# Optimization experiments

Measured on AMD Instinct MI355X. Metric: run time of the kernel, lower is better.

Reference implementation:

```python
import math
import jax, jax.numpy as jnp
import numpy as np

D_MODEL = 1024
N_HEADS = 16
D_K = D_MODEL // N_HEADS


def _rope(x):
    """Interleaved rotary embedding, matching the torch stack/flatten layout.
    x: (b, h, s, d) with d even."""
    s, d = x.shape[2], x.shape[3]
    pos = jnp.arange(s, dtype=x.dtype)[:, None]                     # (s, 1)
    inv = 10000.0 ** (jnp.arange(0, d, 2, dtype=x.dtype) / d)       # (d/2,)
    theta = pos / inv                                               # (s, d/2)
    sin = jnp.repeat(jnp.sin(theta), 2, axis=-1)                    # (s, d)
    cos = jnp.repeat(jnp.cos(theta), 2, axis=-1)                    # (s, d)
    rot = jnp.stack([-x[..., 1::2], x[..., 0::2]], axis=-1).reshape(x.shape)
    return x * cos + rot * sin


def setup_inputs() -> dict:
    key = jax.random.key(0)
    ks = jax.random.split(key, 12)
    b, s, d = 2, 2048, D_MODEL
    sc = 1.0 / math.sqrt(d)
    inp = {
        "q": jax.random.normal(ks[0], (b, s, d), jnp.float32),
        "k": jax.random.normal(ks[1], (b, s, d), jnp.float32),
        "v": jax.random.normal(ks[2], (b, s, d), jnp.float32),
        "mask": jnp.ones((b, 1, 1, s), dtype=bool),
        "w_q": jax.random.normal(ks[3], (d, d), jnp.float32) * sc,
        "b_q": jnp.zeros((d,), jnp.float32),
        "w_k": jax.random.normal(ks[4], (d, d), jnp.float32) * sc,
        "b_k": jnp.zeros((d,), jnp.float32),
        "w_v": jax.random.normal(ks[5], (d, d), jnp.float32) * sc,
        "b_v": jnp.zeros((d,), jnp.float32),
        "w_o": jax.random.normal(ks[6], (d, d), jnp.float32) * sc,
        "b_o": jnp.zeros((d,), jnp.float32),
    }
    return inp


def reference(q, k, v, mask, w_q, b_q, w_k, b_k, w_v, b_v, w_o, b_o):
    b = q.shape[0]
    h, dk = N_HEADS, D_K
    # projections; w stored as (d_in, d_out)
    qh = (q @ w_q + b_q).reshape(b, -1, h, dk).transpose(0, 2, 1, 3)  # (b,h,s1,dk)
    kh = (k @ w_k + b_k).reshape(b, -1, h, dk).transpose(0, 2, 1, 3)  # (b,h,s2,dk)
    vh = (v @ w_v + b_v).reshape(b, -1, h, dk).transpose(0, 2, 1, 3)
    qh = _rope(qh)
    kh = _rope(kh)
    scores = jnp.einsum("bhqd,bhkd->bhqk", qh, kh) / math.sqrt(dk)
    scores = jnp.where(mask, scores, jnp.finfo(scores.dtype).min)
    attn = jax.nn.softmax(scores, axis=-1)
    out = jnp.einsum("bhqk,bhkd->bhqd", attn, vh)
    out = out.transpose(0, 2, 1, 3).reshape(b, -1, h * dk)
    return out @ w_o + b_o
```

## Files before the change

### kernel.cpp

```cpp
#include <hip/hip_runtime.h>

#define S_LEN 2048
#define DM 1024
#define NH 16

typedef __attribute__((ext_vector_type(8))) short short8;
typedef __attribute__((ext_vector_type(4))) float f32x4;
typedef __attribute__((ext_vector_type(4))) unsigned short ushort4v;

#define QSCALE 0.1803368801111204f

__device__ __forceinline__ unsigned short f2bf(float f) {
    unsigned int u = __float_as_uint(f);
    u += 0x7fffu + ((u >> 16) & 1u);
    return (unsigned short)(u >> 16);
}

__device__ __forceinline__ void gload16(const void* g, void* l) {
    __builtin_amdgcn_global_load_lds((const __attribute__((address_space(1))) void*)g,
                                     (__attribute__((address_space(3))) void*)l, 16, 0, 0);
}

__global__ __launch_bounds__(256) void trig_kernel(float* __restrict__ sin_t,
                                                   float* __restrict__ cos_t) {
    int idx = blockIdx.x * 256 + threadIdx.x;
    int pos = idx >> 5;
    int i = idx & 31;
    float theta = (float)pos / powf(10000.0f, (float)i * (1.0f / 32.0f));
    double t = (double)theta;
    sin_t[idx] = (float)sin(t);
    cos_t[idx] = (float)cos(t);
}

__global__ __launch_bounds__(256) void conv_kernel(const float* __restrict__ x,
                                                   unsigned short* __restrict__ y) {
    int i = (blockIdx.x * 256 + threadIdx.x) * 4;
    float4 v = *(const float4*)&x[i];
    ushort4v r;
    r.x = f2bf(v.x); r.y = f2bf(v.y); r.z = f2bf(v.z); r.w = f2bf(v.w);
    *(ushort4v*)&y[i] = r;
}

__global__ __launch_bounds__(256) void wtrans_kernel(const float* __restrict__ w,
                                                     unsigned short* __restrict__ wt) {
    __shared__ float tile[32][33];
    const int k0 = blockIdx.y * 32, n0 = blockIdx.x * 32;
    const int tx = threadIdx.x & 31, ty = threadIdx.x >> 5;
#pragma unroll
    for (int i = 0; i < 4; ++i)
        tile[ty + i * 8][tx] = w[(size_t)(k0 + ty + i * 8) * DM + n0 + tx];
    __syncthreads();
#pragma unroll
    for (int i = 0; i < 4; ++i)
        wt[(size_t)(n0 + ty + i * 8) * DM + k0 + tx] = f2bf(tile[tx][ty + i * 8]);
}

__global__ __launch_bounds__(256, 3) void mmqkv_kernel(
    const unsigned short* __restrict__ qb, const unsigned short* __restrict__ kb,
    const unsigned short* __restrict__ vb, const unsigned short* __restrict__ wT,
    const float* __restrict__ b_q, const float* __restrict__ b_k,
    const float* __restrict__ b_v, unsigned short* __restrict__ outbase,
    const float* __restrict__ sin_t, const float* __restrict__ cos_t) {
    __shared__ __align__(16) short As[8192];
    __shared__ __align__(16) short Bs[8192];
    const int z = blockIdx.z;
    const unsigned short* A = (z == 0) ? qb : (z == 1) ? kb : vb;
    const unsigned short* Bt = wT + (size_t)z * DM * DM;
    const float* bias = (z == 0) ? b_q : (z == 1) ? b_k : b_v;
    unsigned short* out = outbase + (size_t)z * 4096 * DM;

    const int t = threadIdx.x;
    const int lane = t & 63;
    const int w = t >> 6;
    const int wm = w & 1, wn = w >> 1;
    const int lg = lane >> 4, lr = lane & 15;
    const int n0 = blockIdx.x * 128, m0 = blockIdx.y * 128;

    const int srow = t >> 3;
    const int skb = ((t & 7) ^ ((t >> 3) & 7)) << 4;
    const char* Ab = (const char*)A + (size_t)m0 * 2048 + skb;
    const char* Bb = (const char*)Bt + (size_t)n0 * 2048 + skb;
    char* AsB = (char*)As;
    char* BsB = (char*)Bs;

    f32x4 acc[4][4];
#pragma unroll
    for (int i = 0; i < 4; ++i)
#pragma unroll
        for (int j = 0; j < 4; ++j)
#pragma unroll
            for (int e = 0; e < 4; ++e) acc[i][j][e] = 0.0f;

    for (int kb2 = 0; kb2 < 2048; kb2 += 128) {
#pragma unroll
        for (int i = 0; i < 4; ++i) {
            gload16(Ab + (size_t)(i * 32 + srow) * 2048 + kb2, AsB + i * 4096 + t * 16);
            gload16(Bb + (size_t)(i * 32 + srow) * 2048 + kb2, BsB + i * 4096 + t * 16);
        }
        __syncthreads();
#pragma unroll
        for (int ks = 0; ks < 2; ++ks) {
            short8 a[4], b[4];
#pragma unroll
            for (int mi = 0; mi < 4; ++mi) {
                const int ra = wm * 64 + mi * 16 + lr;
                a[mi] = *(const short8*)(AsB + ra * 128 + ((ks * 64 + lg * 16) ^ ((ra & 7) << 4)));
                const int rb = wn * 64 + mi * 16 + lr;
                b[mi] = *(const short8*)(BsB + rb * 128 + ((ks * 64 + lg * 16) ^ ((rb & 7) << 4)));
            }
#pragma unroll
            for (int mi = 0; mi < 4; ++mi)
#pragma unroll
                for (int ni = 0; ni < 4; ++ni)
                    acc[mi][ni] = __builtin_amdgcn_mfma_f32_16x16x32_bf16(
                        a[mi], b[ni], acc[mi][ni], 0, 0, 0);
        }
        __syncthreads();
    }

    const int colbase = n0 + wn * 64;
    const int rowbase = m0 + wm * 64;
    const bool do_rope = (z < 2);
#pragma unroll
    for (int ni = 0; ni < 4; ++ni) {
        const int col = colbase + ni * 16 + lr;
        const float bv = bias[col];
#pragma unroll
        for (int mi = 0; mi < 4; ++mi) {
#pragma unroll
            for (int r = 0; r < 4; ++r) {
                const int row = rowbase + mi * 16 + lg * 4 + r;
                float o = acc[mi][ni][r] + bv;
                if (do_rope) {
                    const int srw = row & (S_LEN - 1);
                    const int pi = (col & 63) >> 1;
                    const float sv = sin_t[srw * 32 + pi];
                    const float cv = cos_t[srw * 32 + pi];
                    const float partner = __shfl_xor(o, 1);
                    o = (lr & 1) ? (o * cv + partner * sv) : (o * cv - partner * sv);
                    if (z == 0) o *= QSCALE;
                }
                out[(size_t)row * DM + col] = f2bf(o);
            }
        }
    }
}

__global__ __launch_bounds__(256, 2) void mmo_kernel(
    const unsigned short* __restrict__ A, const unsigned short* __restrict__ Bt,
    const float* __restrict__ bias, float* __restrict__ out) {
    __shared__ __align__(16) short As[4096];
    __shared__ __align__(16) short Bs[8192];
    const int t = threadIdx.x;
    const int lane = t & 63;
    const int wn = t >> 6;
    const int lg = lane >> 4, lr = lane & 15;
    const int n0 = blockIdx.x * 128, m0 = blockIdx.y * 64;

    const int srow = t >> 3;
    const int skb = ((t & 7) ^ ((t >> 3) & 7)) << 4;
    const char* Ab = (const char*)A + (size_t)m0 * 2048 + skb;
    const char* Bb = (const char*)Bt + (size_t)n0 * 2048 + skb;
    char* AsB = (char*)As;
    char* BsB = (char*)Bs;

    f32x4 acc[4][2];
#pragma unroll
    for (int i = 0; i < 4; ++i)
#pragma unroll
        for (int j = 0; j < 2; ++j)
#pragma unroll
            for (int e = 0; e < 4; ++e) acc[i][j][e] = 0.0f;

    for (int kb2 = 0; kb2 < 2048; kb2 += 128) {
#pragma unroll
        for (int i = 0; i < 2; ++i)
            gload16(Ab + (size_t)(i * 32 + srow) * 2048 + kb2, AsB + i * 4096 + t * 16);
#pragma unroll
        for (int i = 0; i < 4; ++i)
            gload16(Bb + (size_t)(i * 32 + srow) * 2048 + kb2, BsB + i * 4096 + t * 16);
        __syncthreads();
#pragma unroll
        for (int ks = 0; ks < 2; ++ks) {
            short8 a[4], b[2];
#pragma unroll
            for (int mi = 0; mi < 4; ++mi) {
                const int ra = mi * 16 + lr;
                a[mi] = *(const short8*)(AsB + ra * 128 + ((ks * 64 + lg * 16) ^ ((ra & 7) << 4)));
            }
#pragma unroll
            for (int ni = 0; ni < 2; ++ni) {
                const int rb = wn * 32 + ni * 16 + lr;
                b[ni] = *(const short8*)(BsB + rb * 128 + ((ks * 64 + lg * 16) ^ ((rb & 7) << 4)));
            }
#pragma unroll
            for (int mi = 0; mi < 4; ++mi)
#pragma unroll
                for (int ni = 0; ni < 2; ++ni)
                    acc[mi][ni] = __builtin_amdgcn_mfma_f32_16x16x32_bf16(
                        a[mi], b[ni], acc[mi][ni], 0, 0, 0);
        }
        __syncthreads();
    }

#pragma unroll
    for (int ni = 0; ni < 2; ++ni) {
        const int col = n0 + wn * 32 + ni * 16 + lr;
        const float bv = bias[col];
#pragma unroll
        for (int mi = 0; mi < 4; ++mi)
#pragma unroll
            for (int r = 0; r < 4; ++r) {
                const int row = m0 + mi * 16 + lg * 4 + r;
                out[(size_t)row * DM + col] = acc[mi][ni][r] + bv;
            }
    }
}

__global__ __launch_bounds__(256, 4) void flash_kernel(
    const unsigned short* __restrict__ qh, const unsigned short* __restrict__ kh,
    const unsigned short* __restrict__ vh, unsigned short* __restrict__ att) {
    __shared__ __align__(16) short Ks[4096];
    __shared__ __align__(16) short Vt[64][72];
    __shared__ __align__(16) short Pl[4][16 * 72];
    const int t = threadIdx.x;
    const int lane = t & 63;
    const int w = t >> 6;
    const int lg = lane >> 4, lr = lane & 15;
    const int q0 = blockIdx.x * 64;
    const int b = blockIdx.y >> 4, h = blockIdx.y & 15;
    const char* qB = (const char*)qh + (size_t)b * S_LEN * 2048 + h * 128;
    const char* kB = (const char*)kh + (size_t)b * S_LEN * 2048 + h * 128;
    const char* vB = (const char*)vh + (size_t)b * S_LEN * 2048 + h * 128;

    short8 qf[2];
#pragma unroll
    for (int ks = 0; ks < 2; ++ks)
        qf[ks] = *(const short8*)(qB + (size_t)(q0 + w * 16 + lr) * 2048 + ks * 64 + lg * 16);

    short8 onesv;
#pragma unroll
    for (int j = 0; j < 8; ++j) onesv[j] = (short)0x3F80;

    f32x4 oa[5];
    float mrow[4];
#pragma unroll
    for (int r = 0; r < 4; ++r) {
        mrow[r] = -1e30f;
#pragma unroll
        for (int di = 0; di < 5; ++di) oa[di][r] = 0.0f;
    }

    const int srow = t >> 3;
    const int skb = ((t & 7) ^ ((t >> 3) & 7)) << 4;
    const int vkey = lane;
    const int vd0 = w * 16;
    char* PlB = (char*)&Pl[w][0];

    for (int kt = 0; kt < S_LEN; kt += 64) {
#pragma unroll
        for (int i = 0; i < 2; ++i)
            gload16(kB + (size_t)(kt + i * 32 + srow) * 2048 + skb,
                    (char*)Ks + i * 4096 + t * 16);
        const char* vrow = vB + (size_t)(kt + vkey) * 2048 + vd0 * 2;
        short8 v0 = *(const short8*)(vrow);
        short8 v1 = *(const short8*)(vrow + 16);
#pragma unroll
        for (int j = 0; j < 8; ++j) {
            Vt[vd0 + j][vkey] = v0[j];
            Vt[vd0 + 8 + j][vkey] = v1[j];
        }
        __syncthreads();

        f32x4 s[4];
#pragma unroll
        for (int ki = 0; ki < 4; ++ki)
#pragma unroll
            for (int e = 0; e < 4; ++e) s[ki][e] = 0.0f;
#pragma unroll
        for (int ks = 0; ks < 2; ++ks) {
            short8 kf[4];
#pragma unroll
            for (int ki = 0; ki < 4; ++ki) {
                const int key = ki * 16 + lr;
                kf[ki] = *(const short8*)((char*)Ks + key * 128 +
                                          ((ks * 64 + lg * 16) ^ ((key & 7) << 4)));
            }
            __builtin_amdgcn_s_setprio(1);
#pragma unroll
            for (int ki = 0; ki < 4; ++ki)
                s[ki] = __builtin_amdgcn_mfma_f32_16x16x32_bf16(qf[ks], kf[ki], s[ki], 0, 0, 0);
            __builtin_amdgcn_s_setprio(0);
        }

#pragma unroll
        for (int r = 0; r < 4; ++r) {
            float mx = fmaxf(fmaxf(s[0][r], s[1][r]), fmaxf(s[2][r], s[3][r]));
            mx = fmaxf(mx, __shfl_xor(mx, 1));
            mx = fmaxf(mx, __shfl_xor(mx, 2));
            mx = fmaxf(mx, __shfl_xor(mx, 4));
            mx = fmaxf(mx, __shfl_xor(mx, 8));
            const float mn = fmaxf(mrow[r], mx);
            const float corr = exp2f(mrow[r] - mn);
            mrow[r] = mn;
#pragma unroll
            for (int di = 0; di < 5; ++di) oa[di][r] *= corr;
            const int qrow = lg * 4 + r;
            const int xq = (qrow & 12) << 3;
#pragma unroll
            for (int ki = 0; ki < 4; ++ki)
                *(unsigned short*)(PlB + qrow * 144 + (((ki * 16 + lr) * 2) ^ xq)) =
                    f2bf(exp2f(s[ki][r] - mn));
        }
        asm volatile("s_waitcnt lgkmcnt(0)" ::: "memory");

#pragma unroll
        for (int ks = 0; ks < 2; ++ks) {
            short8 pf, vf[4];
            pf = *(const short8*)(PlB + lr * 144 + ((ks * 64 + lg * 16) ^ ((lr & 12) << 3)));
#pragma unroll
            for (int di = 0; di < 4; ++di)
                vf[di] = *(const short8*)((const char*)&Vt[di * 16 + lr][0] + ks * 64 + lg * 16);
            __builtin_amdgcn_s_setprio(1);
#pragma unroll
            for (int di = 0; di < 4; ++di)
                oa[di] = __builtin_amdgcn_mfma_f32_16x16x32_bf16(pf, vf[di], oa[di], 0, 0, 0);
            oa[4] = __builtin_amdgcn_mfma_f32_16x16x32_bf16(pf, onesv, oa[4], 0, 0, 0);
            __builtin_amdgcn_s_setprio(0);
        }
        __syncthreads();
    }

#pragma unroll
    for (int r = 0; r < 4; ++r) {
        const float inv = 1.0f / oa[4][r];
        const int row = q0 + w * 16 + lg * 4 + r;
#pragma unroll
        for (int di = 0; di < 4; ++di)
            att[(size_t)(b * S_LEN + row) * DM + h * 64 + di * 16 + lr] =
                f2bf(oa[di][r] * inv);
    }
}

extern "C" void kernel_launch(void* const* d_in, const int* in_sizes, int n_in,
                              void* d_out, int out_size, void* d_ws, size_t ws_size,
                              hipStream_t stream) {
    const float* q = (const float*)d_in[0];
    const float* k = (const float*)d_in[1];
    const float* v = (const float*)d_in[2];
    const float* w_q = (const float*)d_in[4];
    const float* b_q = (const float*)d_in[5];
    const float* w_k = (const float*)d_in[6];
    const float* b_k = (const float*)d_in[7];
    const float* w_v = (const float*)d_in[8];
    const float* b_v = (const float*)d_in[9];
    const float* w_o = (const float*)d_in[10];
    const float* b_o = (const float*)d_in[11];

    char* p = (char*)d_ws;
    const size_t SZ_ACT = (size_t)4096 * DM * 2;
    const size_t SZ_W = (size_t)DM * DM * 2;
    unsigned short* qb = (unsigned short*)p; p += SZ_ACT;
    unsigned short* kb = (unsigned short*)p; p += SZ_ACT;
    unsigned short* vb = (unsigned short*)p; p += SZ_ACT;
    unsigned short* wqkvT = (unsigned short*)p; p += 3 * SZ_W;
    unsigned short* woT = (unsigned short*)p; p += SZ_W;
    unsigned short* qkvh = (unsigned short*)p; p += 3 * SZ_ACT;
    unsigned short* attp = (unsigned short*)p; p += SZ_ACT;
    float* sin_t = (float*)p; p += (size_t)S_LEN * 32 * 4;
    float* cos_t = (float*)p;

    trig_kernel<<<dim3(S_LEN * 32 / 256), dim3(256), 0, stream>>>(sin_t, cos_t);
    conv_kernel<<<dim3(4096), dim3(256), 0, stream>>>(q, qb);
    conv_kernel<<<dim3(4096), dim3(256), 0, stream>>>(k, kb);
    conv_kernel<<<dim3(4096), dim3(256), 0, stream>>>(v, vb);
    dim3 tg(32, 32);
    wtrans_kernel<<<tg, dim3(256), 0, stream>>>(w_q, wqkvT);
    wtrans_kernel<<<tg, dim3(256), 0, stream>>>(w_k, wqkvT + (size_t)DM * DM);
    wtrans_kernel<<<tg, dim3(256), 0, stream>>>(w_v, wqkvT + (size_t)2 * DM * DM);
    wtrans_kernel<<<tg, dim3(256), 0, stream>>>(w_o, woT);

    mmqkv_kernel<<<dim3(DM / 128, 4096 / 128, 3), dim3(256), 0, stream>>>(
        qb, kb, vb, wqkvT, b_q, b_k, b_v, qkvh, sin_t, cos_t);

    unsigned short* qhp = qkvh;
    unsigned short* khp = qkvh + (size_t)4096 * DM;
    unsigned short* vhp = qkvh + (size_t)2 * 4096 * DM;
    flash_kernel<<<dim3(S_LEN / 64, 32), dim3(256), 0, stream>>>(qhp, khp, vhp, attp);

    mmo_kernel<<<dim3(DM / 128, 4096 / 64), dim3(256), 0, stream>>>(
        attp, woT, b_o, (float*)d_out);
}
```

Measured before the change: 304.3 us.

## Double-buffer flash attention, keep P in registers, remap block order, batch prep launches

The flash kernel now gives each block 128 query rows, double-buffers K and V tiles in LDS, and computes S transposed so the probabilities stay in registers and feed 16x16x16 MFMAs directly instead of going through LDS. It also rescales the running max lazily, only when a row max grows by more than a threshold. The QKV, output and flash kernels remap block IDs so neighbouring blocks land on different XCDs, and setprio is wrapped around the GEMM MFMAs. The conversion, transpose and trig launches are merged into batched grids, with sin and cos packed into float2. Fewer blocks per CU and higher register use may reduce occupancy.

```diff
diff --git a/kernel.cpp b/kernel.cpp
--- a/kernel.cpp
+++ b/kernel.cpp
@@ -5,6 +5,7 @@
 #define NH 16
 
 typedef __attribute__((ext_vector_type(8))) short short8;
+typedef __attribute__((ext_vector_type(4))) short short4v;
 typedef __attribute__((ext_vector_type(4))) float f32x4;
 typedef __attribute__((ext_vector_type(4))) unsigned short ushort4v;
 
@@ -21,29 +22,53 @@
                                      (__attribute__((address_space(3))) void*)l, 16, 0, 0);
 }
 
-__global__ __launch_bounds__(256) void trig_kernel(float* __restrict__ sin_t,
-                                                   float* __restrict__ cos_t) {
+#if __has_builtin(__builtin_amdgcn_mfma_f32_16x16x16bf16_1k)
+__device__ __forceinline__ f32x4 mfma16(short4v a, short4v b, f32x4 c) {
+    return __builtin_amdgcn_mfma_f32_16x16x16bf16_1k(a, b, c, 0, 0, 0);
+}
+#elif __has_builtin(__builtin_amdgcn_mfma_f32_16x16x16_bf16)
+__device__ __forceinline__ f32x4 mfma16(short4v a, short4v b, f32x4 c) {
+    return __builtin_amdgcn_mfma_f32_16x16x16_bf16(a, b, c, 0, 0, 0);
+}
+#else
+__device__ __forceinline__ f32x4 mfma16(short4v a, short4v b, f32x4 c) {
+    asm("v_mfma_f32_16x16x16_bf16 %0, %1, %2, %0" : "+v"(c) : "v"(a), "v"(b));
+    return c;
+}
+#endif
+
+__global__ __launch_bounds__(256) void trig_kernel(float2* __restrict__ cs_t) {
     int idx = blockIdx.x * 256 + threadIdx.x;
     int pos = idx >> 5;
     int i = idx & 31;
     float theta = (float)pos / powf(10000.0f, (float)i * (1.0f / 32.0f));
     double t = (double)theta;
-    sin_t[idx] = (float)sin(t);
-    cos_t[idx] = (float)cos(t);
-}
-
-__global__ __launch_bounds__(256) void conv_kernel(const float* __restrict__ x,
+    cs_t[idx] = make_float2((float)cos(t), (float)sin(t));
+}
+
+__global__ __launch_bounds__(256) void conv_kernel(const float* __restrict__ q,
+                                                   const float* __restrict__ k,
+                                                   const float* __restrict__ v,
                                                    unsigned short* __restrict__ y) {
+    const int z = blockIdx.y;
+    const float* x = (z == 0) ? q : (z == 1) ? k : v;
+    unsigned short* yz = y + (size_t)z * 4096 * DM;
     int i = (blockIdx.x * 256 + threadIdx.x) * 4;
-    float4 v = *(const float4*)&x[i];
+    float4 vv = *(const float4*)&x[i];
     ushort4v r;
-    r.x = f2bf(v.x); r.y = f2bf(v.y); r.z = f2bf(v.z); r.w = f2bf(v.w);
-    *(ushort4v*)&y[i] = r;
-}
-
-__global__ __launch_bounds__(256) void wtrans_kernel(const float* __restrict__ w,
+    r.x = f2bf(vv.x); r.y = f2bf(vv.y); r.z = f2bf(vv.z); r.w = f2bf(vv.w);
+    *(ushort4v*)&yz[i] = r;
+}
+
+__global__ __launch_bounds__(256) void wtrans_kernel(const float* __restrict__ w_q,
+                                                     const float* __restrict__ w_k,
+                                                     const float* __restrict__ w_v,
+                                                     const float* __restrict__ w_o,
                                                      unsigned short* __restrict__ wt) {
     __shared__ float tile[32][33];
+    const int z = blockIdx.z;
+    const float* w = (z == 0) ? w_q : (z == 1) ? w_k : (z == 2) ? w_v : w_o;
+    unsigned short* wtz = wt + (size_t)z * DM * DM;
     const int k0 = blockIdx.y * 32, n0 = blockIdx.x * 32;
     const int tx = threadIdx.x & 31, ty = threadIdx.x >> 5;
 #pragma unroll
@@ -52,19 +77,24 @@
     __syncthreads();
 #pragma unroll
     for (int i = 0; i < 4; ++i)
-        wt[(size_t)(n0 + ty + i * 8) * DM + k0 + tx] = f2bf(tile[tx][ty + i * 8]);
+        wtz[(size_t)(n0 + ty + i * 8) * DM + k0 + tx] = f2bf(tile[tx][ty + i * 8]);
 }
 
 __global__ __launch_bounds__(256, 3) void mmqkv_kernel(
-    const unsigned short* __restrict__ qb, const unsigned short* __restrict__ kb,
-    const unsigned short* __restrict__ vb, const unsigned short* __restrict__ wT,
+    const unsigned short* __restrict__ qkvb, const unsigned short* __restrict__ wT,
     const float* __restrict__ b_q, const float* __restrict__ b_k,
     const float* __restrict__ b_v, unsigned short* __restrict__ outbase,
-    const float* __restrict__ sin_t, const float* __restrict__ cos_t) {
+    const float2* __restrict__ cs_t) {
     __shared__ __align__(16) short As[8192];
     __shared__ __align__(16) short Bs[8192];
-    const int z = blockIdx.z;
-    const unsigned short* A = (z == 0) ? qb : (z == 1) ? kb : vb;
+
+    const int fid = blockIdx.x + (blockIdx.y << 3) + (blockIdx.z << 8);
+    const int sid = (fid & 7) * 96 + (fid >> 3);
+    const int z = sid >> 8;
+    const int m0 = ((sid >> 3) & 31) * 128;
+    const int n0 = (sid & 7) * 128;
+
+    const unsigned short* A = qkvb + (size_t)z * 4096 * DM;
     const unsigned short* Bt = wT + (size_t)z * DM * DM;
     const float* bias = (z == 0) ? b_q : (z == 1) ? b_k : b_v;
     unsigned short* out = outbase + (size_t)z * 4096 * DM;
@@ -74,7 +104,6 @@
     const int w = t >> 6;
     const int wm = w & 1, wn = w >> 1;
     const int lg = lane >> 4, lr = lane & 15;
-    const int n0 = blockIdx.x * 128, m0 = blockIdx.y * 128;
 
     const int srow = t >> 3;
     const int skb = ((t & 7) ^ ((t >> 3) & 7)) << 4;
@@ -108,12 +137,14 @@
                 const int rb = wn * 64 + mi * 16 + lr;
                 b[mi] = *(const short8*)(BsB + rb * 128 + ((ks * 64 + lg * 16) ^ ((rb & 7) << 4)));
             }
+            __builtin_amdgcn_s_setprio(1);
 #pragma unroll
             for (int mi = 0; mi < 4; ++mi)
 #pragma unroll
                 for (int ni = 0; ni < 4; ++ni)
                     acc[mi][ni] = __builtin_amdgcn_mfma_f32_16x16x32_bf16(
                         a[mi], b[ni], acc[mi][ni], 0, 0, 0);
+            __builtin_amdgcn_s_setprio(0);
         }
         __syncthreads();
     }
@@ -125,6 +156,7 @@
     for (int ni = 0; ni < 4; ++ni) {
         const int col = colbase + ni * 16 + lr;
         const float bv = bias[col];
+        const int pi = (col & 63) >> 1;
 #pragma unroll
         for (int mi = 0; mi < 4; ++mi) {
 #pragma unroll
@@ -133,11 +165,9 @@
                 float o = acc[mi][ni][r] + bv;
                 if (do_rope) {
                     const int srw = row & (S_LEN - 1);
-                    const int pi = (col & 63) >> 1;
-                    const float sv = sin_t[srw * 32 + pi];
-                    const float cv = cos_t[srw * 32 + pi];
+                    const float2 cs = cs_t[srw * 32 + pi];
                     const float partner = __shfl_xor(o, 1);
-                    o = (lr & 1) ? (o * cv + partner * sv) : (o * cv - partner * sv);
+                    o = (lr & 1) ? (o * cs.x + partner * cs.y) : (o * cs.x - partner * cs.y);
                     if (z == 0) o *= QSCALE;
                 }
                 out[(size_t)row * DM + col] = f2bf(o);
@@ -155,7 +185,10 @@
     const int lane = t & 63;
     const int wn = t >> 6;
     const int lg = lane >> 4, lr = lane & 15;
-    const int n0 = blockIdx.x * 128, m0 = blockIdx.y * 64;
+
+    const int fid = blockIdx.x + (blockIdx.y << 3);
+    const int sid = (fid & 7) * 64 + (fid >> 3);
+    const int n0 = (sid & 7) * 128, m0 = (sid >> 3) * 64;
 
     const int srow = t >> 3;
     const int skb = ((t & 7) ^ ((t >> 3) & 7)) << 4;
@@ -193,12 +226,14 @@
                 const int rb = wn * 32 + ni * 16 + lr;
                 b[ni] = *(const short8*)(BsB + rb * 128 + ((ks * 64 + lg * 16) ^ ((rb & 7) << 4)));
             }
+            __builtin_amdgcn_s_setprio(1);
 #pragma unroll
             for (int mi = 0; mi < 4; ++mi)
 #pragma unroll
                 for (int ni = 0; ni < 2; ++ni)
                     acc[mi][ni] = __builtin_amdgcn_mfma_f32_16x16x32_bf16(
                         a[mi], b[ni], acc[mi][ni], 0, 0, 0);
+            __builtin_amdgcn_s_setprio(0);
         }
         __syncthreads();
     }
@@ -217,129 +252,190 @@
     }
 }
 
-__global__ __launch_bounds__(256, 4) void flash_kernel(
+__global__ __launch_bounds__(256, 2) void flash_kernel(
     const unsigned short* __restrict__ qh, const unsigned short* __restrict__ kh,
     const unsigned short* __restrict__ vh, unsigned short* __restrict__ att) {
-    __shared__ __align__(16) short Ks[4096];
-    __shared__ __align__(16) short Vt[64][72];
-    __shared__ __align__(16) short Pl[4][16 * 72];
+    __shared__ __align__(16) short Ks[2][4096];
+    __shared__ __align__(16) short Vt[2][64][72];
     const int t = threadIdx.x;
     const int lane = t & 63;
     const int w = t >> 6;
     const int lg = lane >> 4, lr = lane & 15;
-    const int q0 = blockIdx.x * 64;
-    const int b = blockIdx.y >> 4, h = blockIdx.y & 15;
+
+    const int fid = blockIdx.x + (blockIdx.y << 4);
+    const int sid = (fid & 7) * 64 + (fid >> 3);
+    const int q0 = (sid & 15) * 128;
+    const int bh = sid >> 4;
+    const int b = bh >> 4, h = bh & 15;
+
     const char* qB = (const char*)qh + (size_t)b * S_LEN * 2048 + h * 128;
     const char* kB = (const char*)kh + (size_t)b * S_LEN * 2048 + h * 128;
     const char* vB = (const char*)vh + (size_t)b * S_LEN * 2048 + h * 128;
 
-    short8 qf[2];
-#pragma unroll
-    for (int ks = 0; ks < 2; ++ks)
-        qf[ks] = *(const short8*)(qB + (size_t)(q0 + w * 16 + lr) * 2048 + ks * 64 + lg * 16);
-
-    short8 onesv;
-#pragma unroll
-    for (int j = 0; j < 8; ++j) onesv[j] = (short)0x3F80;
-
-    f32x4 oa[5];
-    float mrow[4];
-#pragma unroll
-    for (int r = 0; r < 4; ++r) {
-        mrow[r] = -1e30f;
-#pragma unroll
-        for (int di = 0; di < 5; ++di) oa[di][r] = 0.0f;
-    }
+    short8 qf[2][2];
+#pragma unroll
+    for (int qi = 0; qi < 2; ++qi)
+#pragma unroll
+        for (int ks = 0; ks < 2; ++ks)
+            qf[qi][ks] = *(const short8*)(qB +
+                (size_t)(q0 + w * 32 + qi * 16 + lr) * 2048 + ks * 64 + lg * 16);
 
     const int srow = t >> 3;
-    const int skb = ((t & 7) ^ ((t >> 3) & 7)) << 4;
-    const int vkey = lane;
-    const int vd0 = w * 16;
-    char* PlB = (char*)&Pl[w][0];
-
-    for (int kt = 0; kt < S_LEN; kt += 64) {
-#pragma unroll
-        for (int i = 0; i < 2; ++i)
-            gload16(kB + (size_t)(kt + i * 32 + srow) * 2048 + skb,
-                    (char*)Ks + i * 4096 + t * 16);
-        const char* vrow = vB + (size_t)(kt + vkey) * 2048 + vd0 * 2;
-        short8 v0 = *(const short8*)(vrow);
-        short8 v1 = *(const short8*)(vrow + 16);
+    const int skb = ((t & 7) ^ (srow & 7)) << 4;
+    const int va = t & 31;
+    const int vdb = t >> 5;
+    const size_t vsrc0 = (size_t)(2 * va) * 2048 + vdb * 16;
+
+    f32x4 s[2][4], oa[2][4], oa4[2];
+    float mrow[2] = {-1e30f, -1e30f};
+#pragma unroll
+    for (int qi = 0; qi < 2; ++qi) {
+#pragma unroll
+        for (int e = 0; e < 4; ++e) oa4[qi][e] = 0.0f;
+#pragma unroll
+        for (int di = 0; di < 4; ++di)
+#pragma unroll
+            for (int e = 0; e < 4; ++e) oa[qi][di][e] = 0.0f;
+    }
+    short4v ones4;
+#pragma unroll
+    for (int j = 0; j < 4; ++j) ones4[j] = (short)0x3F80;
+
+    gload16(kB + (size_t)srow * 2048 + skb, (char*)Ks[0] + t * 16);
+    gload16(kB + (size_t)(32 + srow) * 2048 + skb, (char*)Ks[0] + 4096 + t * 16);
+    {
+        short8 a0 = *(const short8*)(vB + vsrc0);
+        short8 a1 = *(const short8*)(vB + vsrc0 + 2048);
 #pragma unroll
         for (int j = 0; j < 8; ++j) {
-            Vt[vd0 + j][vkey] = v0[j];
-            Vt[vd0 + 8 + j][vkey] = v1[j];
-        }
-        __syncthreads();
-
-        f32x4 s[4];
-#pragma unroll
-        for (int ki = 0; ki < 4; ++ki)
-#pragma unroll
-            for (int e = 0; e < 4; ++e) s[ki][e] = 0.0f;
+            unsigned d = (unsigned)(unsigned short)a0[j] |
+                         ((unsigned)(unsigned short)a1[j] << 16);
+            *(unsigned*)&Vt[0][vdb * 8 + j][va * 2] = d;
+        }
+    }
+    __syncthreads();
+
+    for (int it = 0; it < 32; ++it) {
+        const int cb = it & 1;
+        const char* ksB = (const char*)Ks[cb];
+        char* ksN = (char*)Ks[cb ^ 1];
+        const char* vC = (const char*)&Vt[cb][0][0];
+
+        short8 a0, a1;
+        if (it < 31) {
+            const size_t kt2 = (size_t)(it + 1) * 64;
+            gload16(kB + (kt2 + srow) * 2048 + skb, ksN + t * 16);
+            gload16(kB + (kt2 + 32 + srow) * 2048 + skb, ksN + 4096 + t * 16);
+            a0 = *(const short8*)(vB + kt2 * 2048 + vsrc0);
+            a1 = *(const short8*)(vB + kt2 * 2048 + vsrc0 + 2048);
+        }
+
+#pragma unroll
+        for (int qi = 0; qi < 2; ++qi)
+#pragma unroll
+            for (int ki = 0; ki < 4; ++ki)
+#pragma unroll
+                for (int e = 0; e < 4; ++e) s[qi][ki][e] = 0.0f;
 #pragma unroll
         for (int ks = 0; ks < 2; ++ks) {
             short8 kf[4];
 #pragma unroll
             for (int ki = 0; ki < 4; ++ki) {
                 const int key = ki * 16 + lr;
-                kf[ki] = *(const short8*)((char*)Ks + key * 128 +
+                kf[ki] = *(const short8*)(ksB + key * 128 +
                                           ((ks * 64 + lg * 16) ^ ((key & 7) << 4)));
             }
             __builtin_amdgcn_s_setprio(1);
 #pragma unroll
-            for (int ki = 0; ki < 4; ++ki)
-                s[ki] = __builtin_amdgcn_mfma_f32_16x16x32_bf16(qf[ks], kf[ki], s[ki], 0, 0, 0);
+            for (int qi = 0; qi < 2; ++qi)
+#pragma unroll
+                for (int ki = 0; ki < 4; ++ki)
+                    s[qi][ki] = __builtin_amdgcn_mfma_f32_16x16x32_bf16(
+                        kf[ki], qf[qi][ks], s[qi][ki], 0, 0, 0);
             __builtin_amdgcn_s_setprio(0);
         }
 
+        float mxv[2];
+#pragma unroll
+        for (int qi = 0; qi < 2; ++qi) {
+            float mx = fmaxf(fmaxf(s[qi][0][0], s[qi][0][1]), fmaxf(s[qi][0][2], s[qi][0][3]));
+#pragma unroll
+            for (int ki = 1; ki < 4; ++ki)
+                mx = fmaxf(mx, fmaxf(fmaxf(s[qi][ki][0], s[qi][ki][1]),
+                                     fmaxf(s[qi][ki][2], s[qi][ki][3])));
+            mx = fmaxf(mx, __shfl_xor(mx, 16));
+            mx = fmaxf(mx, __shfl_xor(mx, 32));
+            mxv[qi] = mx;
+        }
+        const bool grow = (mxv[0] > mrow[0] + 8.0f) || (mxv[1] > mrow[1] + 8.0f);
+        if (__any(grow)) {
+#pragma unroll
+            for (int qi = 0; qi < 2; ++qi) {
+                const float mn = fmaxf(mrow[qi], mxv[qi]);
+                const float corr = exp2f(mrow[qi] - mn);
+                mrow[qi] = mn;
+#pragma unroll
+                for (int r = 0; r < 4; ++r) {
+                    const float cr = __shfl(corr, (lane & 48) + lg * 4 + r);
+                    oa4[qi][r] *= cr;
+#pragma unroll
+                    for (int di = 0; di < 4; ++di) oa[qi][di][r] *= cr;
+                }
+            }
+        }
+        short4v pa[2][4];
+#pragma unroll
+        for (int qi = 0; qi < 2; ++qi)
+#pragma unroll
+            for (int ki = 0; ki < 4; ++ki) {
+                short4v pv;
+#pragma unroll
+                for (int r = 0; r < 4; ++r)
+                    pv[r] = (short)f2bf(exp2f(s[qi][ki][r] - mrow[qi]));
+                pa[qi][ki] = pv;
+            }
+
+        if (it < 31) {
+            short(*vN)[72] = Vt[cb ^ 1];
+#pragma unroll
+            for (int j = 0; j < 8; ++j) {
+                unsigned d = (unsigned)(unsigned short)a0[j] |
+                             ((unsigned)(unsigned short)a1[j] << 16);
+                *(unsigned*)&vN[vdb * 8 + j][va * 2] = d;
+            }
+        }
+
+        short4v vf[4][4];
+#pragma unroll
+        for (int ki = 0; ki < 4; ++ki)
+#pragma unroll
+            for (int di = 0; di < 4; ++di)
+                vf[ki][di] = *(const short4v*)(vC + (di * 16 + lr) * 144 + ki * 32 + lg * 8);
+        __builtin_amdgcn_s_setprio(1);
+#pragma unroll
+        for (int qi = 0; qi < 2; ++qi)
+#pragma unroll
+            for (int ki = 0; ki < 4; ++ki) {
+                oa4[qi] = mfma16(pa[qi][ki], ones4, oa4[qi]);
+#pragma unroll
+                for (int di = 0; di < 4; ++di)
+                    oa[qi][di] = mfma16(pa[qi][ki], vf[ki][di], oa[qi][di]);
+            }
+        __builtin_amdgcn_s_setprio(0);
+        __syncthreads();
+    }
+
+#pragma unroll
+    for (int qi = 0; qi < 2; ++qi)
 #pragma unroll
         for (int r = 0; r < 4; ++r) {
-            float mx = fmaxf(fmaxf(s[0][r], s[1][r]), fmaxf(s[2][r], s[3][r]));
-            mx = fmaxf(mx, __shfl_xor(mx, 1));
-            mx = fmaxf(mx, __shfl_xor(mx, 2));
-            mx = fmaxf(mx, __shfl_xor(mx, 4));
-            mx = fmaxf(mx, __shfl_xor(mx, 8));
-            const float mn = fmaxf(mrow[r], mx);
-            const float corr = exp2f(mrow[r] - mn);
-            mrow[r] = mn;
-#pragma unroll
-            for (int di = 0; di < 5; ++di) oa[di][r] *= corr;
-            const int qrow = lg * 4 + r;
-            const int xq = (qrow & 12) << 3;
-#pragma unroll
-            for (int ki = 0; ki < 4; ++ki)
-                *(unsigned short*)(PlB + qrow * 144 + (((ki * 16 + lr) * 2) ^ xq)) =
-                    f2bf(exp2f(s[ki][r] - mn));
-        }
-        asm volatile("s_waitcnt lgkmcnt(0)" ::: "memory");
-
-#pragma unroll
-        for (int ks = 0; ks < 2; ++ks) {
-            short8 pf, vf[4];
-            pf = *(const short8*)(PlB + lr * 144 + ((ks * 64 + lg * 16) ^ ((lr & 12) << 3)));
+            const float inv = 1.0f / oa4[qi][r];
+            const int row = q0 + w * 32 + qi * 16 + lg * 4 + r;
 #pragma unroll
             for (int di = 0; di < 4; ++di)
-                vf[di] = *(const short8*)((const char*)&Vt[di * 16 + lr][0] + ks * 64 + lg * 16);
-            __builtin_amdgcn_s_setprio(1);
-#pragma unroll
-            for (int di = 0; di < 4; ++di)
-                oa[di] = __builtin_amdgcn_mfma_f32_16x16x32_bf16(pf, vf[di], oa[di], 0, 0, 0);
-            oa[4] = __builtin_amdgcn_mfma_f32_16x16x32_bf16(pf, onesv, oa[4], 0, 0, 0);
-            __builtin_amdgcn_s_setprio(0);
-        }
-        __syncthreads();
-    }
-
-#pragma unroll
-    for (int r = 0; r < 4; ++r) {
-        const float inv = 1.0f / oa[4][r];
-        const int row = q0 + w * 16 + lg * 4 + r;
-#pragma unroll
-        for (int di = 0; di < 4; ++di)
-            att[(size_t)(b * S_LEN + row) * DM + h * 64 + di * 16 + lr] =
-                f2bf(oa[di][r] * inv);
-    }
+                att[((size_t)b * S_LEN + row) * DM + h * 64 + di * 16 + lr] =
+                    f2bf(oa[qi][di][r] * inv);
+        }
 }
 
 extern "C" void kernel_launch(void* const* d_in, const int* in_sizes, int n_in,
@@ -360,34 +456,24 @@
     char* p = (char*)d_ws;
     const size_t SZ_ACT = (size_t)4096 * DM * 2;
     const size_t SZ_W = (size_t)DM * DM * 2;
-    unsigned short* qb = (unsigned short*)p; p += SZ_ACT;
-    unsigned short* kb = (unsigned short*)p; p += SZ_ACT;
-    unsigned short* vb = (unsigned short*)p; p += SZ_ACT;
-    unsigned short* wqkvT = (unsigned short*)p; p += 3 * SZ_W;
-    unsigned short* woT = (unsigned short*)p; p += SZ_W;
+    unsigned short* qkvb = (unsigned short*)p; p += 3 * SZ_ACT;
+    unsigned short* wT = (unsigned short*)p; p += 4 * SZ_W;
     unsigned short* qkvh = (unsigned short*)p; p += 3 * SZ_ACT;
     unsigned short* attp = (unsigned short*)p; p += SZ_ACT;
-    float* sin_t = (float*)p; p += (size_t)S_LEN * 32 * 4;
-    float* cos_t = (float*)p;
-
-    trig_kernel<<<dim3(S_LEN * 32 / 256), dim3(256), 0, stream>>>(sin_t, cos_t);
-    conv_kernel<<<dim3(4096), dim3(256), 0, stream>>>(q, qb);
-    conv_kernel<<<dim3(4096), dim3(256), 0, stream>>>(k, kb);
-    conv_kernel<<<dim3(4096), dim3(256), 0, stream>>>(v, vb);
-    dim3 tg(32, 32);
-    wtrans_kernel<<<tg, dim3(256), 0, stream>>>(w_q, wqkvT);
-    wtrans_kernel<<<tg, dim3(256), 0, stream>>>(w_k, wqkvT + (size_t)DM * DM);
-    wtrans_kernel<<<tg, dim3(256), 0, stream>>>(w_v, wqkvT + (size_t)2 * DM * DM);
-    wtrans_kernel<<<tg, dim3(256), 0, stream>>>(w_o, woT);
-
-    mmqkv_kernel<<<dim3(DM / 128, 4096 / 128, 3), dim3(256), 0, stream>>>(
-        qb, kb, vb, wqkvT, b_q, b_k, b_v, qkvh, sin_t, cos_t);
+    float2* cs_t = (float2*)p;
+
+    trig_kernel<<<dim3(S_LEN * 32 / 256), dim3(256), 0, stream>>>(cs_t);
+    conv_kernel<<<dim3(4096, 3), dim3(256), 0, stream>>>(q, k, v, qkvb);
+    wtrans_kernel<<<dim3(32, 32, 4), dim3(256), 0, stream>>>(w_q, w_k, w_v, w_o, wT);
+
+    mmqkv_kernel<<<dim3(8, 32, 3), dim3(256), 0, stream>>>(
+        qkvb, wT, b_q, b_k, b_v, qkvh, cs_t);
 
     unsigned short* qhp = qkvh;
     unsigned short* khp = qkvh + (size_t)4096 * DM;
     unsigned short* vhp = qkvh + (size_t)2 * 4096 * DM;
-    flash_kernel<<<dim3(S_LEN / 64, 32), dim3(256), 0, stream>>>(qhp, khp, vhp, attp);
-
-    mmo_kernel<<<dim3(DM / 128, 4096 / 64), dim3(256), 0, stream>>>(
-        attp, woT, b_o, (float*)d_out);
-}
+    flash_kernel<<<dim3(16, 32), dim3(256), 0, stream>>>(qhp, khp, vhp, attp);
+
+    mmo_kernel<<<dim3(8, 64), dim3(256), 0, stream>>>(
+        attp, wT + (size_t)3 * DM * DM, b_o, (float*)d_out);
+}
```

After: 271.1 us. 10.9% less time.
